# Kernel tuning notes

Hardware: AMD Instinct MI355X
Metric: run time of the kernel (lower is better)

The kernel has to match this reference:

```python
import jax, jax.numpy as jnp
import numpy as np

B, S, D = 2, 2048, 1024
H, DK = 16, 64            # n_heads, d_k = d_model // n_heads
EXP = 4                   # pattern-separation expand_factor
ED = DK * EXP             # expanded_dim = 256
TOPK = 32                 # top-k kept after ReLU expansion
ALPHA = 0.05
TNT = 1.0                 # trace_norm_target


def setup_inputs() -> dict:
    key = jax.random.key(0)
    ks = jax.random.split(key, 8)
    sc = 1.0 / np.sqrt(D)
    x = jax.random.normal(ks[0], (B, S, D), jnp.float32)
    W_q = jax.random.normal(ks[1], (D, D), jnp.float32) * sc
    W_k = jax.random.normal(ks[2], (D, D), jnp.float32) * sc
    W_v = jax.random.normal(ks[3], (D, D), jnp.float32) * sc
    W_o = jax.random.normal(ks[4], (D, D), jnp.float32) * sc
    # trace buffers (non-zero so the trace read path actually matters)
    traces = jax.random.normal(ks[5], (H, DK, DK), jnp.float32) * 0.02
    value_traces = jax.random.normal(ks[6], (H, ED, DK), jnp.float32) * 0.02
    # frozen random expansion projection (dentate gyrus), W / sqrt(d_k)
    W_expand = jax.random.normal(ks[7], (DK, ED), jnp.float32) / np.sqrt(DK)
    return dict(x=x, W_q=W_q, W_k=W_k, W_v=W_v, W_o=W_o,
                traces=traces, value_traces=value_traces, W_expand=W_expand)


def _eff_alpha(T):
    # alpha / (1 + ||T_h||_F / trace_norm_target), shape (1, H, 1, 1)
    norms = jnp.sqrt(jnp.sum(T * T, axis=(1, 2)))
    return (ALPHA / (1.0 + norms / TNT)).reshape(1, -1, 1, 1)


def _forward(x, W_q, W_k, W_v, W_o, traces, value_traces, W_expand):
    b, s, d = x.shape
    def proj(W):
        return jnp.einsum('bsd,de->bse', x, W).reshape(b, s, H, DK).transpose(0, 2, 1, 3)
    Q, K, V = proj(W_q), proj(W_k), proj(W_v)  # (B, H, S, DK)

    scores = jnp.einsum('bhqd,bhkd->bhqk', Q, K)
    # score trace bias: alpha_eff * (Q @ T @ K^T)
    QT = jnp.einsum('bhqd,hde->bhqe', Q, traces)
    trace_scores = jnp.einsum('bhqe,bhke->bhqk', QT, K)
    scores = (scores + _eff_alpha(traces) * trace_scores) / np.sqrt(DK)
    A = jax.nn.softmax(scores, axis=-1)
    out = jnp.einsum('bhqk,bhkd->bhqd', A, V)

    # value trace read with use_key_q shift: address with previous token's Q
    Q_addr = jnp.concatenate([jnp.zeros_like(Q[:, :, :1, :]), Q[:, :, :-1, :]], axis=2)
    # pattern separation: frozen random expansion + ReLU + top-k sparsify
    Q_exp = jax.nn.relu(jnp.einsum('bhsd,de->bhse', Q_addr, W_expand))  # (B,H,S,ED)
    kth = jax.lax.top_k(Q_exp, TOPK)[0][..., -1:]
    Q_sparse = jnp.where(Q_exp >= kth, Q_exp, 0.0)  # == scatter of top-k vals (ties at 0 contribute 0)
    stored = jnp.einsum('bhse,hed->bhsd', Q_sparse, value_traces)
    out = out + _eff_alpha(value_traces) * stored

    out = out.transpose(0, 2, 1, 3).reshape(b, s, d)
    return jnp.einsum('bsd,de->bse', out, W_o)


def reference(x, W_q, W_k, W_v, W_o, traces, value_traces, W_expand):
    return _forward(x, W_q, W_k, W_v, W_o, traces, value_traces, W_expand)
```

## Files before the change

### kernel.cpp

```cpp
#include <hip/hip_runtime.h>
#include <stdint.h>

#define Bn 2
#define Sn 2048
#define Dn 1024
#define Hn 16
#define DKn 64
#define EDn 256

typedef __attribute__((ext_vector_type(8))) short bvec8;
typedef __attribute__((ext_vector_type(4))) float fvec4;

#define MFMA(a, b, c) __builtin_amdgcn_mfma_f32_16x16x32_bf16(a, b, c, 0, 0, 0)

__device__ __forceinline__ float b2f(unsigned short u) {
  return __uint_as_float(((unsigned)u) << 16);
}
__device__ __forceinline__ unsigned short f2b(float x) {
  unsigned u = __float_as_uint(x);
  u += 0x7fffu + ((u >> 16) & 1u);
  return (unsigned short)(u >> 16);
}
__device__ __forceinline__ void g2l(const unsigned short* g, unsigned short* l) {
  __builtin_amdgcn_global_load_lds(
      (const __attribute__((address_space(1))) void*)g,
      (__attribute__((address_space(3))) void*)l, 16, 0, 0);
}

__global__ __launch_bounds__(256) void k_alphas(
    const float* __restrict__ traces, const float* __restrict__ vtr,
    float* __restrict__ alphas) {
  int blk = blockIdx.x;
  const float* base;
  int n;
  if (blk < 16) { base = traces + blk * DKn * DKn; n = DKn * DKn; }
  else          { base = vtr + (blk - 16) * EDn * DKn; n = EDn * DKn; }
  float s = 0.f;
  for (int i = threadIdx.x; i < n; i += 256) { float v = base[i]; s += v * v; }
  __shared__ float red[256];
  red[threadIdx.x] = s;
  __syncthreads();
  for (int off = 128; off > 0; off >>= 1) {
    if (threadIdx.x < off) red[threadIdx.x] += red[threadIdx.x + off];
    __syncthreads();
  }
  if (threadIdx.x == 0) alphas[blk] = 0.05f / (1.f + sqrtf(red[0]));
}

__global__ __launch_bounds__(256) void k_trW(
    const float* __restrict__ w0, const float* __restrict__ w1,
    const float* __restrict__ w2, const float* __restrict__ w3,
    unsigned short* __restrict__ dst) {
  int z = blockIdx.z;
  const float* src = (z == 0) ? w0 : ((z == 1) ? w1 : ((z == 2) ? w2 : w3));
  unsigned short* d = dst + (size_t)z * Dn * Dn;
  __shared__ unsigned short Tl[64][72];
  int tid = threadIdx.x;
  int k0 = blockIdx.y * 64, n0 = blockIdx.x * 64;
#pragma unroll
  for (int i = 0; i < 4; ++i) {
    int q = tid + 256 * i;
    int kr = q >> 4, c4 = q & 15;
    float4 v = *(const float4*)&src[(size_t)(k0 + kr) * Dn + n0 + 4 * c4];
    ushort4 u;
    u.x = f2b(v.x); u.y = f2b(v.y); u.z = f2b(v.z); u.w = f2b(v.w);
    *(ushort4*)&Tl[kr][4 * c4] = u;
  }
  __syncthreads();
#pragma unroll
  for (int i = 0; i < 4; ++i) {
    int q = tid + 256 * i;
    int nr = q >> 4, c4 = q & 15;
    ushort4 u;
    u.x = Tl[4 * c4 + 0][nr]; u.y = Tl[4 * c4 + 1][nr];
    u.z = Tl[4 * c4 + 2][nr]; u.w = Tl[4 * c4 + 3][nr];
    *(ushort4*)&d[(size_t)(n0 + nr) * Dn + k0 + 4 * c4] = u;
  }
}

__global__ __launch_bounds__(256) void k_mkM(const float* __restrict__ tr,
                                             const float* __restrict__ alph,
                                             unsigned short* __restrict__ Mt) {
  int h = blockIdx.x;
  float a = alph[h] * 0.125f;
  const float* th = tr + (size_t)h * DKn * DKn;
  unsigned short* mh = Mt + (size_t)h * DKn * DKn;
  for (int i = threadIdx.x; i < DKn * DKn; i += 256) {
    int e = i >> 6, k = i & 63;
    float v = a * th[(size_t)k * DKn + e] + ((e == k) ? 0.125f : 0.f);
    mh[i] = f2b(v);
  }
}

__global__ __launch_bounds__(256) void k_trE(const float* __restrict__ Wexp,
                                             unsigned short* __restrict__ WexpT) {
  int e0 = blockIdx.x * 64;
  __shared__ unsigned short Tl[64][72];
  int tid = threadIdx.x;
#pragma unroll
  for (int i = 0; i < 4; ++i) {
    int q = tid + 256 * i;
    int dr = q >> 4, c4 = q & 15;
    float4 v = *(const float4*)&Wexp[(size_t)dr * EDn + e0 + 4 * c4];
    ushort4 u;
    u.x = f2b(v.x); u.y = f2b(v.y); u.z = f2b(v.z); u.w = f2b(v.w);
    *(ushort4*)&Tl[dr][4 * c4] = u;
  }
  __syncthreads();
#pragma unroll
  for (int i = 0; i < 4; ++i) {
    int q = tid + 256 * i;
    int er = q >> 4, c4 = q & 15;
    ushort4 u;
    u.x = Tl[4 * c4 + 0][er]; u.y = Tl[4 * c4 + 1][er];
    u.z = Tl[4 * c4 + 2][er]; u.w = Tl[4 * c4 + 3][er];
    *(ushort4*)&WexpT[(size_t)(e0 + er) * DKn + 4 * c4] = u;
  }
}

__global__ __launch_bounds__(256) void k_trVT(const float* __restrict__ vtr,
                                              unsigned short* __restrict__ VTt) {
  int e0 = blockIdx.x * 64;
  int h = blockIdx.y;
  const float* src = vtr + (size_t)h * EDn * DKn;
  unsigned short* dst = VTt + (size_t)h * DKn * EDn;
  __shared__ unsigned short Tl[64][72];
  int tid = threadIdx.x;
#pragma unroll
  for (int i = 0; i < 4; ++i) {
    int q = tid + 256 * i;
    int er = q >> 4, c4 = q & 15;
    float4 v = *(const float4*)&src[(size_t)(e0 + er) * DKn + 4 * c4];
    ushort4 u;
    u.x = f2b(v.x); u.y = f2b(v.y); u.z = f2b(v.z); u.w = f2b(v.w);
    *(ushort4*)&Tl[er][4 * c4] = u;
  }
  __syncthreads();
#pragma unroll
  for (int i = 0; i < 4; ++i) {
    int q = tid + 256 * i;
    int dr = q >> 4, c4 = q & 15;
    ushort4 u;
    u.x = Tl[4 * c4 + 0][dr]; u.y = Tl[4 * c4 + 1][dr];
    u.z = Tl[4 * c4 + 2][dr]; u.w = Tl[4 * c4 + 3][dr];
    *(ushort4*)&dst[(size_t)dr * EDn + e0 + 4 * c4] = u;
  }
}

__global__ __launch_bounds__(256) void k_xb(const float* __restrict__ x,
                                            unsigned short* __restrict__ xb) {
  size_t i = ((size_t)blockIdx.x * 256 + threadIdx.x) * 4;
  float4 v = *(const float4*)&x[i];
  ushort4 u;
  u.x = f2b(v.x); u.y = f2b(v.y); u.z = f2b(v.z); u.w = f2b(v.w);
  *(ushort4*)&xb[i] = u;
}

template <int MODE>
__global__ __launch_bounds__(256) void k_gemm(
    const unsigned short* __restrict__ Ab, const float* __restrict__ Af,
    const unsigned short* __restrict__ BtBase, unsigned short* __restrict__ Qb,
    unsigned short* __restrict__ Kb, unsigned short* __restrict__ VtOut,
    float* __restrict__ Cout) {
  const int z = (MODE == 0) ? blockIdx.z : 0;
  const unsigned short* Bt = BtBase + (size_t)z * Dn * Dn;
  __shared__ unsigned short As[128 * 32];
  __shared__ unsigned short Bs[128 * 32];
  const int tid = threadIdx.x;
  const int w = tid >> 6, lane = tid & 63, qd = lane >> 4, cc = lane & 15;
  const int m0 = blockIdx.y * 128, n0 = blockIdx.x * 128;
  const int mW = 64 * (w >> 1), nW = 64 * (w & 1);
  const int srow = lane >> 2;
  const int schk = 8 * ((lane & 3) ^ (srow & 3));
  const int r0 = 32 * w + srow, r1 = r0 + 16;
  fvec4 acc[4][4];
#pragma unroll
  for (int i = 0; i < 4; ++i)
#pragma unroll
    for (int j = 0; j < 4; ++j) acc[i][j] = (fvec4){0.f, 0.f, 0.f, 0.f};

  for (int k0 = 0; k0 < Dn; k0 += 32) {
    if (MODE == 0) {
      g2l(&Ab[(size_t)(m0 + r0) * Dn + k0 + schk], &As[1024 * w]);
      g2l(&Ab[(size_t)(m0 + r1) * Dn + k0 + schk], &As[1024 * w + 512]);
    } else {
#pragma unroll
      for (int i = 0; i < 4; ++i) {
        int q = tid + 256 * i;
        int row = q >> 3, c4 = q & 7;
        float4 v = *(const float4*)&Af[(size_t)(m0 + row) * Dn + k0 + 4 * c4];
        ushort4 u;
        u.x = f2b(v.x); u.y = f2b(v.y); u.z = f2b(v.z); u.w = f2b(v.w);
        *(ushort4*)&As[row * 32 + 8 * ((c4 >> 1) ^ (row & 3)) + 4 * (c4 & 1)] =
            u;
      }
    }
    g2l(&Bt[(size_t)(n0 + r0) * Dn + k0 + schk], &Bs[1024 * w]);
    g2l(&Bt[(size_t)(n0 + r1) * Dn + k0 + schk], &Bs[1024 * w + 512]);
    __syncthreads();
    bvec8 af[4], bf[4];
#pragma unroll
    for (int i = 0; i < 4; ++i) {
      int ra = mW + 16 * i + cc;
      af[i] = *(const bvec8*)&As[ra * 32 + 8 * (qd ^ (ra & 3))];
      int rb = nW + 16 * i + cc;
      bf[i] = *(const bvec8*)&Bs[rb * 32 + 8 * (qd ^ (rb & 3))];
    }
#pragma unroll
    for (int i = 0; i < 4; ++i)
#pragma unroll
      for (int j = 0; j < 4; ++j) acc[i][j] = MFMA(af[i], bf[j], acc[i][j]);
    __syncthreads();
  }
#pragma unroll
  for (int i = 0; i < 4; ++i)
#pragma unroll
    for (int j = 0; j < 4; ++j) {
      int rowb = m0 + mW + 16 * i + 4 * qd;
      int col = n0 + nW + 16 * j + cc;
      if (MODE == 0) {
        int b = rowb >> 11, s = rowb & 2047;
        int h = col >> 6, dk = col & 63;
        if (z == 2) {
          ushort4 u;
          u.x = f2b(acc[i][j][0]); u.y = f2b(acc[i][j][1]);
          u.z = f2b(acc[i][j][2]); u.w = f2b(acc[i][j][3]);
          *(ushort4*)&VtOut[(((size_t)(b * Hn + h)) * DKn + dk) * Sn + s] = u;
        } else {
          unsigned short* Cb = (z == 0) ? Qb : Kb;
#pragma unroll
          for (int r = 0; r < 4; ++r)
            Cb[(((size_t)(b * Hn + h)) * Sn + s + r) * DKn + dk] =
                f2b(acc[i][j][r]);
        }
      } else {
#pragma unroll
        for (int r = 0; r < 4; ++r)
          Cout[(size_t)(rowb + r) * Dn + col] = acc[i][j][r];
      }
    }
}

__global__ __launch_bounds__(256, 2) void k_pattsep(
    const unsigned short* __restrict__ Qb,
    const unsigned short* __restrict__ WexpT,
    const unsigned short* __restrict__ VTt,
    const float* __restrict__ alphas, float* __restrict__ AT) {
  __shared__ uint4 Wl4[2048];
  __shared__ uint4 Vl4[2048];
  __shared__ uint4 Ps4[4][256];
  const int tile = blockIdx.x, bh = blockIdx.y;
  const int b = bh >> 4, h = bh & 15;
  const int tid = threadIdx.x;
  const int w = tid >> 6, lane = tid & 63, qd = lane >> 4, cc = lane & 15;
  const float avt = alphas[16 + h];

  const uint4* wsrc = (const uint4*)WexpT;
  const uint4* vsrc = (const uint4*)(VTt + (size_t)h * DKn * EDn);
  for (int i = tid; i < 2048; i += 256) {
    int e = i >> 3, c = i & 7;
    Wl4[e * 8 + (c ^ (e & 7))] = wsrc[i];
    int d = i >> 5, c2 = i & 31;
    Vl4[d * 32 + (c2 ^ (d & 7))] = vsrc[i];
  }
  __syncthreads();

  const unsigned short* Wls = (const unsigned short*)Wl4;
  const unsigned short* Vls = (const unsigned short*)Vl4;
  unsigned short* Pw = (unsigned short*)Ps4[w];

  for (int rg = 0; rg < 2; ++rg) {
    const int s0 = tile * 128 + w * 32 + rg * 16;
    bvec8 aq0 = {}, aq1 = {};
    const int srow = s0 + cc;
    if (srow > 0) {
      const unsigned short* qp = Qb + ((size_t)bh * Sn + srow - 1) * DKn;
      aq0 = *(const bvec8*)&qp[8 * qd];
      aq1 = *(const bvec8*)&qp[32 + 8 * qd];
    }
    fvec4 E[16];
#pragma unroll
    for (int j = 0; j < 16; ++j) {
      const int e = 16 * j + cc;
      const unsigned short* wr = Wls + e * 64;
      bvec8 b0 = *(const bvec8*)&wr[8 * (qd ^ (e & 7))];
      bvec8 b1 = *(const bvec8*)&wr[8 * ((4 + qd) ^ (e & 7))];
      fvec4 zv = {0.f, 0.f, 0.f, 0.f};
      zv = MFMA(aq0, b0, zv);
      E[j] = MFMA(aq1, b1, zv);
    }
#pragma unroll
    for (int j = 0; j < 16; ++j)
#pragma unroll
      for (int r = 0; r < 4; ++r) E[j][r] = fmaxf(E[j][r], 0.f);

    float thr[4];
#pragma unroll
    for (int r = 0; r < 4; ++r) {
      unsigned cur = 0u;
      bool done = false;
      for (int bit = 30; bit >= 0; --bit) {
        unsigned cand = cur | (1u << bit);
        float t = __uint_as_float(cand);
        int cnt = 0;
#pragma unroll
        for (int j = 0; j < 16; ++j) cnt += (E[j][r] >= t) ? 1 : 0;
        cnt += __shfl_xor(cnt, 1);
        cnt += __shfl_xor(cnt, 2);
        cnt += __shfl_xor(cnt, 4);
        cnt += __shfl_xor(cnt, 8);
        if (!done && cnt >= 32) {
          cur = cand;
          if (cnt == 32) done = true;
        }
        if (__all(done)) break;
      }
      thr[r] = __uint_as_float(cur);
    }

    fvec4 acc2[4];
#pragma unroll
    for (int j2 = 0; j2 < 4; ++j2) acc2[j2] = (fvec4){0.f, 0.f, 0.f, 0.f};

#pragma unroll
    for (int half = 0; half < 2; ++half) {
#pragma unroll
      for (int j = 0; j < 8; ++j) {
        const int jj = j + 8 * half;
#pragma unroll
        for (int r = 0; r < 4; ++r) {
          float v = E[jj][r];
          bool sel = (v >= thr[r]) && (v > 0.f);
          int row = 4 * qd + r;
          int s = 16 * j + cc;
          int ch = (s >> 3) ^ (row & 7);
          Pw[row * 128 + ch * 8 + (s & 7)] = sel ? f2b(v) : (unsigned short)0;
        }
      }
#pragma unroll
      for (int j2 = 0; j2 < 4; ++j2) {
        const int d = 16 * j2 + cc;
        const unsigned short* vr = Vls + d * 256;
#pragma unroll
        for (int c = 0; c < 4; ++c) {
          int cg = 4 * (c + 4 * half) + qd;
          bvec8 bv = *(const bvec8*)&vr[8 * (cg ^ (d & 7))];
          int ca = 4 * c + qd;
          bvec8 ap = *(const bvec8*)&Pw[cc * 128 + 8 * (ca ^ (cc & 7))];
          acc2[j2] = MFMA(ap, bv, acc2[j2]);
        }
      }
    }
#pragma unroll
    for (int j2 = 0; j2 < 4; ++j2)
#pragma unroll
      for (int r = 0; r < 4; ++r) {
        int row = s0 + 4 * qd + r;
        AT[((size_t)(b * Sn + row)) * Dn + h * DKn + 16 * j2 + cc] =
            avt * acc2[j2][r];
      }
  }
}

__global__ __launch_bounds__(256) void k_attn(
    const unsigned short* __restrict__ Qb, const unsigned short* __restrict__ Kb,
    const unsigned short* __restrict__ Vt, const unsigned short* __restrict__ Mt,
    float* __restrict__ AT) {
  __shared__ unsigned short Kd[2][64 * 64];
  __shared__ unsigned short Vl[2][64 * 64];
  __shared__ unsigned short Ps[4][16 * 64];
  const int bh = blockIdx.x, qt = blockIdx.y;
  const int b = bh >> 4, h = bh & 15;
  const int tid = threadIdx.x;
  const int w = tid >> 6, lane = tid & 63, qd = lane >> 4, cc = lane & 15;
  const float L2E = 1.4426950408889634f;
  const float NB = 23.083120654223414f;

  const unsigned short* qg = Qb + ((size_t)bh * Sn + qt * 64 + w * 16) * DKn;
  bvec8 a0 = *(const bvec8*)&qg[cc * DKn + 8 * qd];
  bvec8 a1 = *(const bvec8*)&qg[cc * DKn + 32 + 8 * qd];
  const unsigned short* mh = Mt + (size_t)h * DKn * DKn;
  unsigned short* Ksc = Kd[0];
#pragma unroll
  for (int j = 0; j < 4; ++j) {
    bvec8 b0 = *(const bvec8*)&mh[(size_t)(16 * j + cc) * DKn + 8 * qd];
    bvec8 b1 = *(const bvec8*)&mh[(size_t)(16 * j + cc) * DKn + 32 + 8 * qd];
    fvec4 zz = {0.f, 0.f, 0.f, 0.f};
    zz = MFMA(a0, b0, zz);
    zz = MFMA(a1, b1, zz);
#pragma unroll
    for (int r = 0; r < 4; ++r) {
      int qr = 4 * qd + r;
      Ksc[(16 * w + qr) * 64 + 8 * ((2 * j + (cc >> 3)) ^ (qr & 7)) + (cc & 7)] =
          f2b(zz[r]);
    }
  }
  bvec8 aq0 = *(const bvec8*)&Ksc[(16 * w + cc) * 64 + 8 * (qd ^ (cc & 7))];
  bvec8 aq1 =
      *(const bvec8*)&Ksc[(16 * w + cc) * 64 + 8 * ((qd + 4) ^ (cc & 7))];
  asm volatile("s_waitcnt lgkmcnt(0)" ::: "memory");

  float l_s = 0.f;
  fvec4 O[4];
#pragma unroll
  for (int j = 0; j < 4; ++j) O[j] = (fvec4){0.f, 0.f, 0.f, 0.f};

  const int vrow = lane >> 3;
  const int vchk = 8 * ((lane & 7) ^ (vrow & 7));
  const unsigned short* kgb = Kb + (size_t)bh * Sn * DKn;
  const unsigned short* vgb = Vt + (size_t)bh * DKn * Sn;

  g2l(&kgb[(size_t)(16 * w + vrow) * 64 + vchk], &Kd[0][1024 * w]);
  g2l(&kgb[(size_t)(16 * w + 8 + vrow) * 64 + vchk], &Kd[0][1024 * w + 512]);
  g2l(&vgb[(size_t)(16 * w + vrow) * Sn + vchk], &Vl[0][1024 * w]);
  g2l(&vgb[(size_t)(16 * w + 8 + vrow) * Sn + vchk], &Vl[0][1024 * w + 512]);

  const int NT = Sn / 64;
  for (int kt = 0; kt < NT; ++kt) {
    const int buf = kt & 1;
    asm volatile("s_waitcnt vmcnt(0)" ::: "memory");
    __builtin_amdgcn_s_barrier();
    if (kt + 1 < NT) {
      const unsigned short* kg = kgb + (size_t)(kt + 1) * 64 * DKn;
      unsigned short* Kn = Kd[buf ^ 1];
      unsigned short* Vn = Vl[buf ^ 1];
      g2l(&kg[(size_t)(16 * w + vrow) * 64 + vchk], &Kn[1024 * w]);
      g2l(&kg[(size_t)(16 * w + 8 + vrow) * 64 + vchk], &Kn[1024 * w + 512]);
      g2l(&vgb[(size_t)(16 * w + vrow) * Sn + (kt + 1) * 64 + vchk],
          &Vn[1024 * w]);
      g2l(&vgb[(size_t)(16 * w + 8 + vrow) * Sn + (kt + 1) * 64 + vchk],
          &Vn[1024 * w + 512]);
    }
    __builtin_amdgcn_sched_barrier(0);
    const unsigned short* Kc = Kd[buf];
    const unsigned short* Vc = Vl[buf];
    fvec4 sc[4];
#pragma unroll
    for (int j = 0; j < 4; ++j) {
      int rk = 16 * j + cc;
      bvec8 b0 = *(const bvec8*)&Kc[rk * 64 + 8 * (qd ^ (cc & 7))];
      bvec8 b1 = *(const bvec8*)&Kc[rk * 64 + 8 * ((qd + 4) ^ (cc & 7))];
      fvec4 zz = {0.f, 0.f, 0.f, 0.f};
      zz = MFMA(b0, aq0, zz);
      sc[j] = MFMA(b1, aq1, zz);
    }
    unsigned short* Pw = Ps[w];
#pragma unroll
    for (int j = 0; j < 4; ++j) {
      float p0 = __builtin_amdgcn_exp2f(fmaf(sc[j][0], L2E, -NB));
      float p1 = __builtin_amdgcn_exp2f(fmaf(sc[j][1], L2E, -NB));
      float p2 = __builtin_amdgcn_exp2f(fmaf(sc[j][2], L2E, -NB));
      float p3 = __builtin_amdgcn_exp2f(fmaf(sc[j][3], L2E, -NB));
      l_s += (p0 + p1) + (p2 + p3);
      unsigned q01, q23;
      asm("v_cvt_pk_bf16_f32 %0, %1, %2" : "=v"(q01) : "v"(p0), "v"(p1));
      asm("v_cvt_pk_bf16_f32 %0, %1, %2" : "=v"(q23) : "v"(p2), "v"(p3));
      uint2 uu;
      uu.x = q01; uu.y = q23;
      *(uint2*)&Pw[cc * 64 + 4 * ((4 * j + qd) ^ cc)] = uu;
    }
    union U16 { bvec8 v; uint2 u[2]; } U0, U1;
    U0.u[0] = *(const uint2*)&Pw[cc * 64 + 4 * ((2 * qd) ^ cc)];
    U0.u[1] = *(const uint2*)&Pw[cc * 64 + 4 * ((2 * qd + 1) ^ cc)];
    U1.u[0] = *(const uint2*)&Pw[cc * 64 + 4 * ((8 + 2 * qd) ^ cc)];
    U1.u[1] = *(const uint2*)&Pw[cc * 64 + 4 * ((9 + 2 * qd) ^ cc)];
    bvec8 ap0 = U0.v, ap1 = U1.v;
#pragma unroll
    for (int j = 0; j < 4; ++j) {
      int rv = 16 * j + cc;
      bvec8 v0 = *(const bvec8*)&Vc[rv * 64 + 8 * (qd ^ (cc & 7))];
      bvec8 v1 = *(const bvec8*)&Vc[rv * 64 + 8 * ((qd + 4) ^ (cc & 7))];
      O[j] = MFMA(ap0, v0, O[j]);
      O[j] = MFMA(ap1, v1, O[j]);
    }
  }
  l_s += __shfl_xor(l_s, 16);
  l_s += __shfl_xor(l_s, 32);
  float linv = 1.f / l_s;
  float inv[4];
#pragma unroll
  for (int r = 0; r < 4; ++r) inv[r] = __shfl(linv, 4 * qd + r);
#pragma unroll
  for (int j = 0; j < 4; ++j)
#pragma unroll
    for (int r = 0; r < 4; ++r) {
      int row = qt * 64 + w * 16 + 4 * qd + r;
      float* p = AT + ((size_t)(b * Sn + row)) * Dn + h * DKn + 16 * j + cc;
      *p += O[j][r] * inv[r];
    }
}

extern "C" void kernel_launch(void* const* d_in, const int* in_sizes, int n_in,
                              void* d_out, int out_size, void* d_ws,
                              size_t ws_size, hipStream_t stream) {
  const float* x = (const float*)d_in[0];
  const float* Wq = (const float*)d_in[1];
  const float* Wk = (const float*)d_in[2];
  const float* Wv = (const float*)d_in[3];
  const float* Wo = (const float*)d_in[4];
  const float* traces = (const float*)d_in[5];
  const float* vtr = (const float*)d_in[6];
  const float* Wexp = (const float*)d_in[7];

  const size_t NQ = (size_t)Bn * Hn * Sn * DKn;
  unsigned short* Qb = (unsigned short*)d_ws;
  unsigned short* Kb = Qb + NQ;
  unsigned short* Vt = Kb + NQ;
  unsigned short* Wt = Vt + NQ;
  unsigned short* Mt = Wt + NQ;
  unsigned short* WexpT = Mt + 65536;
  unsigned short* VTt = WexpT + 16384;
  float* alph = (float*)(VTt + 262144);
  float* AT = alph + 32;
  unsigned short* xb = (unsigned short*)AT;

  k_alphas<<<32, 256, 0, stream>>>(traces, vtr, alph);
  k_trW<<<dim3(16, 16, 4), 256, 0, stream>>>(Wq, Wk, Wv, Wo, Wt);
  k_mkM<<<16, 256, 0, stream>>>(traces, alph, Mt);
  k_trE<<<4, 256, 0, stream>>>(Wexp, WexpT);
  k_trVT<<<dim3(4, 16), 256, 0, stream>>>(vtr, VTt);
  k_xb<<<4096, 256, 0, stream>>>(x, xb);
  k_gemm<0><<<dim3(8, 32, 3), 256, 0, stream>>>(xb, nullptr, Wt, Qb, Kb, Vt,
                                                nullptr);
  k_pattsep<<<dim3(16, 32), 256, 0, stream>>>(Qb, WexpT, VTt, alph, AT);
  k_attn<<<dim3(32, 32), 256, 0, stream>>>(Qb, Kb, Vt, Mt, AT);
  k_gemm<1><<<dim3(8, 32, 1), 256, 0, stream>>>(
      nullptr, AT, Wt + 3 * (size_t)Dn * Dn, nullptr, nullptr, nullptr,
      (float*)d_out);
}
```

Before: 308.3 us.

## Process two 16-row query fragments per wave in attention kernel

Each wave of the attention kernel now handles 32 query rows as two MFMA fragments instead of 16, so each block covers 128 queries and the grid's query dimension halves. Every K/V tile loaded into LDS is reused for twice as many queries, halving global K/V traffic and the number of block-wide barriers per query. The cost is more accumulator registers per thread, a larger per-wave P staging buffer, and only 512 blocks, which may limit occupancy and wave count on a 256-CU part; launch bounds now request 2 blocks per CU.

```diff
diff --git a/kernel.cpp b/kernel.cpp
--- a/kernel.cpp
+++ b/kernel.cpp
@@ -362,13 +362,13 @@
   }
 }
 
-__global__ __launch_bounds__(256) void k_attn(
+__global__ __launch_bounds__(256, 2) void k_attn(
     const unsigned short* __restrict__ Qb, const unsigned short* __restrict__ Kb,
     const unsigned short* __restrict__ Vt, const unsigned short* __restrict__ Mt,
     float* __restrict__ AT) {
   __shared__ unsigned short Kd[2][64 * 64];
   __shared__ unsigned short Vl[2][64 * 64];
-  __shared__ unsigned short Ps[4][16 * 64];
+  __shared__ unsigned short Ps[4][32 * 64];
   const int bh = blockIdx.x, qt = blockIdx.y;
   const int b = bh >> 4, h = bh & 15;
   const int tid = threadIdx.x;
@@ -376,34 +376,44 @@
   const float L2E = 1.4426950408889634f;
   const float NB = 23.083120654223414f;
 
-  const unsigned short* qg = Qb + ((size_t)bh * Sn + qt * 64 + w * 16) * DKn;
-  bvec8 a0 = *(const bvec8*)&qg[cc * DKn + 8 * qd];
-  bvec8 a1 = *(const bvec8*)&qg[cc * DKn + 32 + 8 * qd];
+  const unsigned short* qg = Qb + ((size_t)bh * Sn + qt * 128 + w * 32) * DKn;
   const unsigned short* mh = Mt + (size_t)h * DKn * DKn;
-  unsigned short* Ksc = Kd[0];
+  unsigned short* Pw = Ps[w];
+  bvec8 mb0[4], mb1[4];
 #pragma unroll
   for (int j = 0; j < 4; ++j) {
-    bvec8 b0 = *(const bvec8*)&mh[(size_t)(16 * j + cc) * DKn + 8 * qd];
-    bvec8 b1 = *(const bvec8*)&mh[(size_t)(16 * j + cc) * DKn + 32 + 8 * qd];
-    fvec4 zz = {0.f, 0.f, 0.f, 0.f};
-    zz = MFMA(a0, b0, zz);
-    zz = MFMA(a1, b1, zz);
-#pragma unroll
-    for (int r = 0; r < 4; ++r) {
-      int qr = 4 * qd + r;
-      Ksc[(16 * w + qr) * 64 + 8 * ((2 * j + (cc >> 3)) ^ (qr & 7)) + (cc & 7)] =
-          f2b(zz[r]);
-    }
-  }
-  bvec8 aq0 = *(const bvec8*)&Ksc[(16 * w + cc) * 64 + 8 * (qd ^ (cc & 7))];
-  bvec8 aq1 =
-      *(const bvec8*)&Ksc[(16 * w + cc) * 64 + 8 * ((qd + 4) ^ (cc & 7))];
-  asm volatile("s_waitcnt lgkmcnt(0)" ::: "memory");
-
-  float l_s = 0.f;
-  fvec4 O[4];
-#pragma unroll
-  for (int j = 0; j < 4; ++j) O[j] = (fvec4){0.f, 0.f, 0.f, 0.f};
+    mb0[j] = *(const bvec8*)&mh[(size_t)(16 * j + cc) * DKn + 8 * qd];
+    mb1[j] = *(const bvec8*)&mh[(size_t)(16 * j + cc) * DKn + 32 + 8 * qd];
+  }
+#pragma unroll
+  for (int f = 0; f < 2; ++f) {
+    bvec8 a0 = *(const bvec8*)&qg[(16 * f + cc) * DKn + 8 * qd];
+    bvec8 a1 = *(const bvec8*)&qg[(16 * f + cc) * DKn + 32 + 8 * qd];
+#pragma unroll
+    for (int j = 0; j < 4; ++j) {
+      fvec4 zz = {0.f, 0.f, 0.f, 0.f};
+      zz = MFMA(a0, mb0[j], zz);
+      zz = MFMA(a1, mb1[j], zz);
+#pragma unroll
+      for (int r = 0; r < 4; ++r) {
+        int qr = 16 * f + 4 * qd + r;
+        Pw[qr * 64 + 8 * ((2 * j + (cc >> 3)) ^ (qr & 7)) + (cc & 7)] =
+            f2b(zz[r]);
+      }
+    }
+  }
+  bvec8 aqA0 = *(const bvec8*)&Pw[cc * 64 + 8 * (qd ^ (cc & 7))];
+  bvec8 aqA1 = *(const bvec8*)&Pw[cc * 64 + 8 * ((qd + 4) ^ (cc & 7))];
+  bvec8 aqB0 = *(const bvec8*)&Pw[(16 + cc) * 64 + 8 * (qd ^ (cc & 7))];
+  bvec8 aqB1 = *(const bvec8*)&Pw[(16 + cc) * 64 + 8 * ((qd + 4) ^ (cc & 7))];
+
+  float lsA = 0.f, lsB = 0.f;
+  fvec4 OA[4], OB[4];
+#pragma unroll
+  for (int j = 0; j < 4; ++j) {
+    OA[j] = (fvec4){0.f, 0.f, 0.f, 0.f};
+    OB[j] = (fvec4){0.f, 0.f, 0.f, 0.f};
+  }
 
   const int vrow = lane >> 3;
   const int vchk = 8 * ((lane & 7) ^ (vrow & 7));
@@ -434,24 +444,26 @@
     __builtin_amdgcn_sched_barrier(0);
     const unsigned short* Kc = Kd[buf];
     const unsigned short* Vc = Vl[buf];
-    fvec4 sc[4];
+    fvec4 sA[4], sB[4];
 #pragma unroll
     for (int j = 0; j < 4; ++j) {
       int rk = 16 * j + cc;
       bvec8 b0 = *(const bvec8*)&Kc[rk * 64 + 8 * (qd ^ (cc & 7))];
       bvec8 b1 = *(const bvec8*)&Kc[rk * 64 + 8 * ((qd + 4) ^ (cc & 7))];
-      fvec4 zz = {0.f, 0.f, 0.f, 0.f};
-      zz = MFMA(b0, aq0, zz);
-      sc[j] = MFMA(b1, aq1, zz);
-    }
-    unsigned short* Pw = Ps[w];
+      fvec4 z0 = {0.f, 0.f, 0.f, 0.f};
+      z0 = MFMA(b0, aqA0, z0);
+      sA[j] = MFMA(b1, aqA1, z0);
+      fvec4 z1 = {0.f, 0.f, 0.f, 0.f};
+      z1 = MFMA(b0, aqB0, z1);
+      sB[j] = MFMA(b1, aqB1, z1);
+    }
 #pragma unroll
     for (int j = 0; j < 4; ++j) {
-      float p0 = __builtin_amdgcn_exp2f(fmaf(sc[j][0], L2E, -NB));
-      float p1 = __builtin_amdgcn_exp2f(fmaf(sc[j][1], L2E, -NB));
-      float p2 = __builtin_amdgcn_exp2f(fmaf(sc[j][2], L2E, -NB));
-      float p3 = __builtin_amdgcn_exp2f(fmaf(sc[j][3], L2E, -NB));
-      l_s += (p0 + p1) + (p2 + p3);
+      float p0 = __builtin_amdgcn_exp2f(fmaf(sA[j][0], L2E, -NB));
+      float p1 = __builtin_amdgcn_exp2f(fmaf(sA[j][1], L2E, -NB));
+      float p2 = __builtin_amdgcn_exp2f(fmaf(sA[j][2], L2E, -NB));
+      float p3 = __builtin_amdgcn_exp2f(fmaf(sA[j][3], L2E, -NB));
+      lsA += (p0 + p1) + (p2 + p3);
       unsigned q01, q23;
       asm("v_cvt_pk_bf16_f32 %0, %1, %2" : "=v"(q01) : "v"(p0), "v"(p1));
       asm("v_cvt_pk_bf16_f32 %0, %1, %2" : "=v"(q23) : "v"(p2), "v"(p3));
@@ -459,34 +471,60 @@
       uu.x = q01; uu.y = q23;
       *(uint2*)&Pw[cc * 64 + 4 * ((4 * j + qd) ^ cc)] = uu;
     }
-    union U16 { bvec8 v; uint2 u[2]; } U0, U1;
-    U0.u[0] = *(const uint2*)&Pw[cc * 64 + 4 * ((2 * qd) ^ cc)];
-    U0.u[1] = *(const uint2*)&Pw[cc * 64 + 4 * ((2 * qd + 1) ^ cc)];
-    U1.u[0] = *(const uint2*)&Pw[cc * 64 + 4 * ((8 + 2 * qd) ^ cc)];
-    U1.u[1] = *(const uint2*)&Pw[cc * 64 + 4 * ((9 + 2 * qd) ^ cc)];
-    bvec8 ap0 = U0.v, ap1 = U1.v;
+#pragma unroll
+    for (int j = 0; j < 4; ++j) {
+      float p0 = __builtin_amdgcn_exp2f(fmaf(sB[j][0], L2E, -NB));
+      float p1 = __builtin_amdgcn_exp2f(fmaf(sB[j][1], L2E, -NB));
+      float p2 = __builtin_amdgcn_exp2f(fmaf(sB[j][2], L2E, -NB));
+      float p3 = __builtin_amdgcn_exp2f(fmaf(sB[j][3], L2E, -NB));
+      lsB += (p0 + p1) + (p2 + p3);
+      unsigned q01, q23;
+      asm("v_cvt_pk_bf16_f32 %0, %1, %2" : "=v"(q01) : "v"(p0), "v"(p1));
+      asm("v_cvt_pk_bf16_f32 %0, %1, %2" : "=v"(q23) : "v"(p2), "v"(p3));
+      uint2 uu;
+      uu.x = q01; uu.y = q23;
+      *(uint2*)&Pw[(16 + cc) * 64 + 4 * ((4 * j + qd) ^ cc)] = uu;
+    }
+    union U16 { bvec8 v; uint2 u[2]; } UA0, UA1, UB0, UB1;
+    UA0.u[0] = *(const uint2*)&Pw[cc * 64 + 4 * ((2 * qd) ^ cc)];
+    UA0.u[1] = *(const uint2*)&Pw[cc * 64 + 4 * ((2 * qd + 1) ^ cc)];
+    UA1.u[0] = *(const uint2*)&Pw[cc * 64 + 4 * ((8 + 2 * qd) ^ cc)];
+    UA1.u[1] = *(const uint2*)&Pw[cc * 64 + 4 * ((9 + 2 * qd) ^ cc)];
+    UB0.u[0] = *(const uint2*)&Pw[(16 + cc) * 64 + 4 * ((2 * qd) ^ cc)];
+    UB0.u[1] = *(const uint2*)&Pw[(16 + cc) * 64 + 4 * ((2 * qd + 1) ^ cc)];
+    UB1.u[0] = *(const uint2*)&Pw[(16 + cc) * 64 + 4 * ((8 + 2 * qd) ^ cc)];
+    UB1.u[1] = *(const uint2*)&Pw[(16 + cc) * 64 + 4 * ((9 + 2 * qd) ^ cc)];
 #pragma unroll
     for (int j = 0; j < 4; ++j) {
       int rv = 16 * j + cc;
       bvec8 v0 = *(const bvec8*)&Vc[rv * 64 + 8 * (qd ^ (cc & 7))];
       bvec8 v1 = *(const bvec8*)&Vc[rv * 64 + 8 * ((qd + 4) ^ (cc & 7))];
-      O[j] = MFMA(ap0, v0, O[j]);
-      O[j] = MFMA(ap1, v1, O[j]);
-    }
-  }
-  l_s += __shfl_xor(l_s, 16);
-  l_s += __shfl_xor(l_s, 32);
-  float linv = 1.f / l_s;
-  float inv[4];
-#pragma unroll
-  for (int r = 0; r < 4; ++r) inv[r] = __shfl(linv, 4 * qd + r);
+      OA[j] = MFMA(UA0.v, v0, OA[j]);
+      OA[j] = MFMA(UA1.v, v1, OA[j]);
+      OB[j] = MFMA(UB0.v, v0, OB[j]);
+      OB[j] = MFMA(UB1.v, v1, OB[j]);
+    }
+  }
+  lsA += __shfl_xor(lsA, 16);
+  lsA += __shfl_xor(lsA, 32);
+  lsB += __shfl_xor(lsB, 16);
+  lsB += __shfl_xor(lsB, 32);
+  float liA = 1.f / lsA, liB = 1.f / lsB;
+  float iA[4], iB[4];
+#pragma unroll
+  for (int r = 0; r < 4; ++r) {
+    iA[r] = __shfl(liA, 4 * qd + r);
+    iB[r] = __shfl(liB, 4 * qd + r);
+  }
 #pragma unroll
   for (int j = 0; j < 4; ++j)
 #pragma unroll
     for (int r = 0; r < 4; ++r) {
-      int row = qt * 64 + w * 16 + 4 * qd + r;
-      float* p = AT + ((size_t)(b * Sn + row)) * Dn + h * DKn + 16 * j + cc;
-      *p += O[j][r] * inv[r];
+      int rowA = qt * 128 + w * 32 + 4 * qd + r;
+      float* pA = AT + ((size_t)(b * Sn + rowA)) * Dn + h * DKn + 16 * j + cc;
+      *pA += OA[j][r] * iA[r];
+      float* pB = pA + 16 * (size_t)Dn;
+      *pB += OB[j][r] * iB[r];
     }
 }
 
@@ -523,7 +561,7 @@
   k_gemm<0><<<dim3(8, 32, 3), 256, 0, stream>>>(xb, nullptr, Wt, Qb, Kb, Vt,
                                                 nullptr);
   k_pattsep<<<dim3(16, 32), 256, 0, stream>>>(Qb, WexpT, VTt, alph, AT);
-  k_attn<<<dim3(32, 32), 256, 0, stream>>>(Qb, Kb, Vt, Mt, AT);
+  k_attn<<<dim3(32, 16), 256, 0, stream>>>(Qb, Kb, Vt, Mt, AT);
   k_gemm<1><<<dim3(8, 32, 1), 256, 0, stream>>>(
       nullptr, AT, Wt + 3 * (size_t)Dn * Dn, nullptr, nullptr, nullptr,
       (float*)d_out);
```

After: 300.9 us. 2.4% less time.
